# Performance work log

Measured on AMD Instinct MI355X. Metric: run time of the kernel, lower is better.

The kernel has to match this reference:

```python
import jax, jax.numpy as jnp
import numpy as np

WIN = 9


def _box_sum(x, win):
    """Windowed sum over the 3 spatial dims of x: [B,1,D,H,W].

    Separable: three 1-D all-ones convolutions give the exact same sums as the
    original dense win^3 ones-kernel conv, in O(win) per voxel instead of O(win^3).
    """
    pad = win // 2
    for axis in range(3):
        kshape = [1, 1, 1, 1, 1]
        kshape[2 + axis] = win
        kernel = jnp.ones(kshape, x.dtype)
        padding = [(0, 0), (0, 0), (0, 0)]
        padding[axis] = (pad, pad)
        x = jax.lax.conv_general_dilated(
            x, kernel, window_strides=(1, 1, 1), padding=padding,
            dimension_numbers=('NCDHW', 'OIDHW', 'NCDHW'))
    return x


def setup_inputs() -> dict:
    key = jax.random.key(0)
    k1, k2 = jax.random.split(key)
    shape = (2, 1, 160, 192, 160)
    y_true = jax.random.normal(k1, shape, dtype=jnp.float32)
    y_pred = jax.random.normal(k2, shape, dtype=jnp.float32)
    return {"y_true": y_true, "y_pred": y_pred}


def reference(y_true, y_pred):
    Ii, Ji = y_true, y_pred
    win_size = WIN ** 3  # 729

    I_sum = _box_sum(Ii, WIN)
    J_sum = _box_sum(Ji, WIN)
    I2_sum = _box_sum(Ii * Ii, WIN)
    J2_sum = _box_sum(Ji * Ji, WIN)
    IJ_sum = _box_sum(Ii * Ji, WIN)

    u_I = I_sum / win_size
    u_J = J_sum / win_size

    cross = IJ_sum - u_J * I_sum - u_I * J_sum + u_I * u_J * win_size
    I_var = I2_sum - 2.0 * u_I * I_sum + u_I * u_I * win_size
    J_var = J2_sum - 2.0 * u_J * J_sum + u_J * u_J * win_size

    cc = cross * cross / (I_var * J_var + 1e-5)
    # torch: cc.mean(dim=(1,2,3)) per batch (leaves last spatial dim), then -cc.mean()
    cc_b = cc.mean(axis=(1, 2, 3))
    return -cc_b.mean()
```

## Files before the change

kernel.cpp:

```cpp
#include <hip/hip_runtime.h>


#define NB 2
#define ND 160
#define NH 192
#define NW 160
#define TH 16
#define TW 16
#define ZC 32
#define NSTEP (ZC + 8)
#define NSUP (NSTEP / 2)
#define NGRID 1200
#define CPX (NGRID / 8)
#define HROWS 25
#define HSTR 20
#define VROWS 17
#define VSTR 24
#define VFSTR (VROWS * VSTR)
#define NTH 256

#define HSWZ(r) ((((r) >> 3) & 3) << 2)

__device__ __forceinline__ float4 f4add(float4 a, float4 b) {
    return make_float4(a.x + b.x, a.y + b.y, a.z + b.z, a.w + b.w);
}
__device__ __forceinline__ float4 f4sub(float4 a, float4 b) {
    return make_float4(a.x - b.x, a.y - b.y, a.z - b.z, a.w - b.w);
}

__device__ __forceinline__ void barw() {
    asm volatile("s_waitcnt lgkmcnt(0)" ::: "memory");
    __builtin_amdgcn_s_barrier();
    asm volatile("" ::: "memory");
}

__global__ __launch_bounds__(NTH) void ncc_main(
        const float* __restrict__ I, const float* __restrict__ J,
        double* __restrict__ gacc) {
    __shared__ float hsum[2][5][HROWS][HSTR];
    __shared__ float vsum[2][5][VROWS][VSTR];
    __shared__ double wred[4];

    const int tid = threadIdx.x;
    const int tx = tid & 15;
    const int ty = tid >> 4;

    const int bid = blockIdx.x;
    const int nid = (bid & 7) * CPX + (bid >> 3);
    const int tile = nid / 10;
    const int rem = nid - tile * 10;
    const int zci = rem >> 1;
    const int bb = rem & 1;
    const int tileW = tile % 10;
    const int tileH = tile / 10;
    const int w0 = tileW * TW;
    const int h0 = tileH * TH;
    const int z0 = zci * ZC;
    const size_t volBase = (size_t)bb * ND * NH * NW;

    const bool bs_on = (tid < 96);
    const int bp = (bs_on && tid >= 48) ? 1 : 0;
    const int b2 = bs_on ? (tid - bp * 48) : 0;
    const int br = b2 >> 1;
    const int bo = b2 & 1;
    const int bh = h0 - 4 + br;
    const bool h_ok = bs_on && bh >= 0 && bh < NH;
    bool wok[4];
    int goff[4];
#pragma unroll
    for (int kk = 0; kk < 4; ++kk) {
        const int w = w0 - 4 + 8 * bo + 4 * kk;
        wok[kk] = (w >= 0) && (w <= NW - 4);
        goff[kk] = bh * NW + w;
    }
    float bI[16], bJ[16];
#pragma unroll
    for (int k = 0; k < 4; ++k) {
        *(float4*)&bI[4 * k] = make_float4(0.f, 0.f, 0.f, 0.f);
        *(float4*)&bJ[4 * k] = make_float4(0.f, 0.f, 0.f, 0.f);
    }

    const bool c_on = (tid >= 96);
    const int cix = c_on ? (tid - 96) : 0;
    const int cp = (cix >= 80) ? 1 : 0;
    const int c2 = cix - cp * 80;
    const int cf = c2 >> 4;
    const int cstrip = (c2 >> 2) & 3;
    const int ccg = c2 & 3;
    const int cr0 = cstrip << 2;
    const int cc0 = ccg << 2;
    float* cdst = &vsum[cp][cf][cr0][cc0];

#define ISSUE(t) do {                                                          \
    const int zt_ = z0 - 4 + 2 * (t) + bp;                                     \
    const bool zok_ = (zt_ >= 0) && (zt_ < ND);                                \
    const size_t zb_ = volBase + (size_t)zt_ * (NH * NW);                      \
    _Pragma("unroll") for (int kk = 0; kk < 4; ++kk) {                         \
        *(float4*)&bI[4 * kk] = make_float4(0.f, 0.f, 0.f, 0.f);               \
        *(float4*)&bJ[4 * kk] = make_float4(0.f, 0.f, 0.f, 0.f);               \
        if (h_ok && zok_ && wok[kk]) {                                         \
            *(float4*)&bI[4 * kk] = *(const float4*)(I + zb_ + goff[kk]);      \
            *(float4*)&bJ[4 * kk] = *(const float4*)(J + zb_ + goff[kk]);      \
        }                                                                      \
    }                                                                          \
} while (0)

#define BSLIDE(EXPR, F) do {                                                   \
    float s_ = EXPR(0);                                                        \
    _Pragma("unroll") for (int k_ = 1; k_ < 9; ++k_) s_ += EXPR(k_);           \
    float o_[8]; o_[0] = s_;                                                   \
    _Pragma("unroll") for (int j_ = 1; j_ < 8; ++j_) {                         \
        s_ += EXPR(j_ + 8) - EXPR(j_ - 1); o_[j_] = s_; }                      \
    *(float4*)&hsum[bp][F][br][(8 * bo) ^ HSWZ(br)]     = *(float4*)&o_[0];    \
    *(float4*)&hsum[bp][F][br][(8 * bo + 4) ^ HSWZ(br)] = *(float4*)&o_[4];    \
} while (0)
#define E_I(k)  bI[k]
#define E_J(k)  bJ[k]
#define E_I2(k) (bI[k] * bI[k])
#define E_J2(k) (bJ[k] * bJ[k])
#define E_IJ(k) (bI[k] * bJ[k])

#define BSTW() do { if (bs_on) {                                               \
    BSLIDE(E_I, 0); BSLIDE(E_J, 1); BSLIDE(E_I2, 2);                           \
    BSLIDE(E_J2, 3); BSLIDE(E_IJ, 4);                                          \
} } while (0)

#define CRD(r) (*(const float4*)&hsum[cp][cf][r][cc0 ^ HSWZ(r)])

#define DO_C() do { if (c_on) {                                                \
    float4 r0v = CRD(cr0 + 0);                                                 \
    float4 r1v = CRD(cr0 + 1);                                                 \
    float4 r2v = CRD(cr0 + 2);                                                 \
    float4 s4 = f4add(f4add(r0v, r1v), r2v);                                   \
    _Pragma("unroll") for (int k = 3; k < 9; ++k)                              \
        s4 = f4add(s4, CRD(cr0 + k));                                          \
    *(float4*)(cdst + 0 * VSTR) = s4;                                          \
    s4 = f4sub(f4add(s4, CRD(cr0 +  9)), r0v);                                 \
    *(float4*)(cdst + 1 * VSTR) = s4;                                          \
    s4 = f4sub(f4add(s4, CRD(cr0 + 10)), r1v);                                 \
    *(float4*)(cdst + 2 * VSTR) = s4;                                          \
    s4 = f4sub(f4add(s4, CRD(cr0 + 11)), r2v);                                 \
    *(float4*)(cdst + 3 * VSTR) = s4;                                          \
} } while (0)

#define DO_D(PL, SLOT, IDX) do {                                               \
    const float* vbase_ = &vsum[PL][0][ty][tx];                                \
    _Pragma("unroll") for (int f = 0; f < 5; ++f) {                            \
        const float v = vbase_[f * VFSTR];                                     \
        acc[f] += v - ring[f][SLOT];                                           \
        ring[f][SLOT] = v;                                                     \
    }                                                                          \
    if ((IDX) >= 8) {                                                          \
        const float Is = acc[0], Js = acc[1];                                  \
        const float I2 = acc[2], J2 = acc[3], IJ = acc[4];                     \
        const float inv = 1.0f / 729.0f;                                       \
        const float uI = Is * inv, uJ = Js * inv;                              \
        const float cross = IJ - uJ * Is - uI * Js + uI * uJ * 729.0f;         \
        const float Iv = I2 - 2.0f * uI * Is + uI * uI * 729.0f;               \
        const float Jv = J2 - 2.0f * uJ * Js + uJ * uJ * 729.0f;               \
        partial += cross * cross / (Iv * Jv + 1e-5f);                          \
    }                                                                          \
} while (0)

    float ring[5][9];
    float acc[5];
#pragma unroll
    for (int f = 0; f < 5; ++f) {
        acc[f] = 0.f;
#pragma unroll
        for (int k = 0; k < 9; ++k) ring[f][k] = 0.f;
    }
    float partial = 0.f;

    ISSUE(0);
    BSTW();
    ISSUE(1);
    barw();

#pragma unroll 1
    for (int ss = 0; ss < 27; ss += 9) {
#pragma unroll
        for (int jj = 0; jj < 9; ++jj) {
            const int s = ss + jj;
            if (s < NSUP) {
                DO_C();
                barw();

                if (s + 1 < NSUP) BSTW();
                if (s + 2 < NSUP) ISSUE(s + 2);
                DO_D(0, (2 * jj) % 9, 2 * s);
                DO_D(1, (2 * jj + 1) % 9, 2 * s + 1);
                barw();
            }
        }
    }

    double dp = (double)partial;
#pragma unroll
    for (int off = 32; off > 0; off >>= 1)
        dp += __shfl_down(dp, off, 64);
    if ((tid & 63) == 0) wred[tid >> 6] = dp;
    __syncthreads();
    if (tid == 0) atomicAdd(gacc, wred[0] + wred[1] + wred[2] + wred[3]);
}

__global__ void ncc_fin(const double* __restrict__ gacc, float* __restrict__ out) {
    out[0] = (float)(-gacc[0] / (double)((long long)NB * ND * NH * NW));
}

extern "C" void kernel_launch(void* const* d_in, const int* in_sizes, int n_in,
                              void* d_out, int out_size, void* d_ws, size_t ws_size,
                              hipStream_t stream) {
    const float* I = (const float*)d_in[0];
    const float* J = (const float*)d_in[1];
    double* ws = (double*)d_ws;

    hipMemsetAsync(d_ws, 0, sizeof(double), stream);

    ncc_main<<<dim3(NGRID), NTH, 0, stream>>>(I, J, ws);
    ncc_fin<<<1, 1, 0, stream>>>(ws, (float*)d_out);
}
```

Baseline: 91.51 us.

## Switch to single-plane pipeline with smaller z-chunks and more blocks

Replaces the two-plane-per-step pipeline with one z-plane per step. The z-chunk shrinks from 32 to 20 and the grid grows from 1200 to 1920 blocks, so there is more block-level parallelism. In exchange, the 8-plane halo is a larger share of each chunk, so more redundant loads and work, and there are twice as many barriers per plane. It also simplifies the covariance algebra (cross = IJ - uI*Js, etc.), which is mathematically equivalent and saves a few flops.

```diff
diff --git a/kernel.cpp b/kernel.cpp
--- a/kernel.cpp
+++ b/kernel.cpp
@@ -7,10 +7,10 @@
 #define NW 160
 #define TH 16
 #define TW 16
-#define ZC 32
+#define ZC 20
 #define NSTEP (ZC + 8)
-#define NSUP (NSTEP / 2)
-#define NGRID 1200
+#define NITER 36
+#define NGRID 1920
 #define CPX (NGRID / 8)
 #define HROWS 25
 #define HSTR 20
@@ -37,8 +37,8 @@
 __global__ __launch_bounds__(NTH) void ncc_main(
         const float* __restrict__ I, const float* __restrict__ J,
         double* __restrict__ gacc) {
-    __shared__ float hsum[2][5][HROWS][HSTR];
-    __shared__ float vsum[2][5][VROWS][VSTR];
+    __shared__ float hsum[5][HROWS][HSTR];
+    __shared__ float vsum[5][VROWS][VSTR];
     __shared__ double wred[4];
 
     const int tid = threadIdx.x;
@@ -47,8 +47,8 @@
 
     const int bid = blockIdx.x;
     const int nid = (bid & 7) * CPX + (bid >> 3);
-    const int tile = nid / 10;
-    const int rem = nid - tile * 10;
+    const int tile = nid >> 4;
+    const int rem = nid & 15;
     const int zci = rem >> 1;
     const int bb = rem & 1;
     const int tileW = tile % 10;
@@ -58,11 +58,9 @@
     const int z0 = zci * ZC;
     const size_t volBase = (size_t)bb * ND * NH * NW;
 
-    const bool bs_on = (tid < 96);
-    const int bp = (bs_on && tid >= 48) ? 1 : 0;
-    const int b2 = bs_on ? (tid - bp * 48) : 0;
-    const int br = b2 >> 1;
-    const int bo = b2 & 1;
+    const bool bs_on = (tid < 48);
+    const int br = tid >> 1;
+    const int bo = tid & 1;
     const int bh = h0 - 4 + br;
     const bool h_ok = bs_on && bh >= 0 && bh < NH;
     bool wok[4];
@@ -80,19 +78,17 @@
         *(float4*)&bJ[4 * k] = make_float4(0.f, 0.f, 0.f, 0.f);
     }
 
-    const bool c_on = (tid >= 96);
+    const bool c_on = (tid >= 96) && (tid < 176);
     const int cix = c_on ? (tid - 96) : 0;
-    const int cp = (cix >= 80) ? 1 : 0;
-    const int c2 = cix - cp * 80;
-    const int cf = c2 >> 4;
-    const int cstrip = (c2 >> 2) & 3;
-    const int ccg = c2 & 3;
+    const int cf = cix >> 4;
+    const int cstrip = (cix >> 2) & 3;
+    const int ccg = cix & 3;
     const int cr0 = cstrip << 2;
     const int cc0 = ccg << 2;
-    float* cdst = &vsum[cp][cf][cr0][cc0];
+    float* cdst = &vsum[cf][cr0][cc0];
 
 #define ISSUE(t) do {                                                          \
-    const int zt_ = z0 - 4 + 2 * (t) + bp;                                     \
+    const int zt_ = z0 - 4 + (t);                                              \
     const bool zok_ = (zt_ >= 0) && (zt_ < ND);                                \
     const size_t zb_ = volBase + (size_t)zt_ * (NH * NW);                      \
     _Pragma("unroll") for (int kk = 0; kk < 4; ++kk) {                         \
@@ -111,8 +107,8 @@
     float o_[8]; o_[0] = s_;                                                   \
     _Pragma("unroll") for (int j_ = 1; j_ < 8; ++j_) {                         \
         s_ += EXPR(j_ + 8) - EXPR(j_ - 1); o_[j_] = s_; }                      \
-    *(float4*)&hsum[bp][F][br][(8 * bo) ^ HSWZ(br)]     = *(float4*)&o_[0];    \
-    *(float4*)&hsum[bp][F][br][(8 * bo + 4) ^ HSWZ(br)] = *(float4*)&o_[4];    \
+    *(float4*)&hsum[F][br][(8 * bo) ^ HSWZ(br)]     = *(float4*)&o_[0];        \
+    *(float4*)&hsum[F][br][(8 * bo + 4) ^ HSWZ(br)] = *(float4*)&o_[4];        \
 } while (0)
 #define E_I(k)  bI[k]
 #define E_J(k)  bJ[k]
@@ -125,7 +121,7 @@
     BSLIDE(E_J2, 3); BSLIDE(E_IJ, 4);                                          \
 } } while (0)
 
-#define CRD(r) (*(const float4*)&hsum[cp][cf][r][cc0 ^ HSWZ(r)])
+#define CRD(r) (*(const float4*)&hsum[cf][r][cc0 ^ HSWZ(r)])
 
 #define DO_C() do { if (c_on) {                                                \
     float4 r0v = CRD(cr0 + 0);                                                 \
@@ -143,8 +139,8 @@
     *(float4*)(cdst + 3 * VSTR) = s4;                                          \
 } } while (0)
 
-#define DO_D(PL, SLOT, IDX) do {                                               \
-    const float* vbase_ = &vsum[PL][0][ty][tx];                                \
+#define DO_D(SLOT, IDX) do {                                                   \
+    const float* vbase_ = &vsum[0][ty][tx];                                    \
     _Pragma("unroll") for (int f = 0; f < 5; ++f) {                            \
         const float v = vbase_[f * VFSTR];                                     \
         acc[f] += v - ring[f][SLOT];                                           \
@@ -155,9 +151,9 @@
         const float I2 = acc[2], J2 = acc[3], IJ = acc[4];                     \
         const float inv = 1.0f / 729.0f;                                       \
         const float uI = Is * inv, uJ = Js * inv;                              \
-        const float cross = IJ - uJ * Is - uI * Js + uI * uJ * 729.0f;         \
-        const float Iv = I2 - 2.0f * uI * Is + uI * uI * 729.0f;               \
-        const float Jv = J2 - 2.0f * uJ * Js + uJ * uJ * 729.0f;               \
+        const float cross = IJ - uI * Js;                                      \
+        const float Iv = I2 - uI * Is;                                         \
+        const float Jv = J2 - uJ * Js;                                         \
         partial += cross * cross / (Iv * Jv + 1e-5f);                          \
     }                                                                          \
 } while (0)
@@ -178,18 +174,17 @@
     barw();
 
 #pragma unroll 1
-    for (int ss = 0; ss < 27; ss += 9) {
+    for (int ss = 0; ss < NITER; ss += 9) {
 #pragma unroll
         for (int jj = 0; jj < 9; ++jj) {
             const int s = ss + jj;
-            if (s < NSUP) {
+            if (s < NSTEP) {
                 DO_C();
                 barw();
 
-                if (s + 1 < NSUP) BSTW();
-                if (s + 2 < NSUP) ISSUE(s + 2);
-                DO_D(0, (2 * jj) % 9, 2 * s);
-                DO_D(1, (2 * jj + 1) % 9, 2 * s + 1);
+                if (s + 1 < NSTEP) BSTW();
+                if (s + 2 < NSTEP) ISSUE(s + 2);
+                DO_D(jj, s);
                 barw();
             }
         }
```

Measured after the change: 257.2 us. 2.81x slower.

## Spread horizontal box-sum work across all waves, one field per thread

Applied to the files above, without the earlier changes.

The horizontal sliding-sum stage is rebalanced so each of the four waves uses 60 lanes, with every thread handling a single field (I, J, I², J², or (I+J)²) over one 24-wide row. The vertical stage likewise uses 40 lanes per wave instead of dedicated warps. IJ is recovered algebraically as ((I+J)² − I² − J²)/2, and the cross and variance formulas are simplified. This balances the stage work across all waves rather than leaving some waves idle, at the cost of redundant global loads per field and some loss of precision from the polarization identity.

```diff
diff --git a/kernel.cpp b/kernel.cpp
--- a/kernel.cpp
+++ b/kernel.cpp
@@ -10,6 +10,7 @@
 #define ZC 32
 #define NSTEP (ZC + 8)
 #define NSUP (NSTEP / 2)
+#define NITER 27
 #define NGRID 1200
 #define CPX (NGRID / 8)
 #define HROWS 25
@@ -42,6 +43,8 @@
     __shared__ double wred[4];
 
     const int tid = threadIdx.x;
+    const int lane = tid & 63;
+    const int wv = tid >> 6;
     const int tx = tid & 15;
     const int ty = tid >> 4;
 
@@ -58,74 +61,75 @@
     const int z0 = zci * ZC;
     const size_t volBase = (size_t)bb * ND * NH * NW;
 
-    const bool bs_on = (tid < 96);
-    const int bp = (bs_on && tid >= 48) ? 1 : 0;
-    const int b2 = bs_on ? (tid - bp * 48) : 0;
-    const int br = b2 >> 1;
-    const int bo = b2 & 1;
-    const int bh = h0 - 4 + br;
+    const bool bs_on = (lane < 60);
+    const int tk = wv * 60 + (bs_on ? lane : 0);
+    const int bpl = tk / 120;
+    const int bf = (tk / 24) % 5;
+    const int brow = tk % 24;
+    const int bh = h0 - 4 + brow;
     const bool h_ok = bs_on && bh >= 0 && bh < NH;
-    bool wok[4];
-    int goff[4];
-#pragma unroll
-    for (int kk = 0; kk < 4; ++kk) {
-        const int w = w0 - 4 + 8 * bo + 4 * kk;
+    const bool isK = (bf == 4);
+    const float* PA = (bf == 1 || bf == 3) ? J : I;
+    bool wok[6];
+    int goff[6];
+#pragma unroll
+    for (int kk = 0; kk < 6; ++kk) {
+        const int w = w0 - 4 + 4 * kk;
         wok[kk] = (w >= 0) && (w <= NW - 4);
         goff[kk] = bh * NW + w;
     }
-    float bI[16], bJ[16];
-#pragma unroll
-    for (int k = 0; k < 4; ++k) {
-        *(float4*)&bI[4 * k] = make_float4(0.f, 0.f, 0.f, 0.f);
-        *(float4*)&bJ[4 * k] = make_float4(0.f, 0.f, 0.f, 0.f);
-    }
-
-    const bool c_on = (tid >= 96);
-    const int cix = c_on ? (tid - 96) : 0;
-    const int cp = (cix >= 80) ? 1 : 0;
-    const int c2 = cix - cp * 80;
+    float bR[24];
+#pragma unroll
+    for (int k = 0; k < 6; ++k) *(float4*)&bR[4 * k] = make_float4(0.f, 0.f, 0.f, 0.f);
+
+    const bool c_on = (lane < 40);
+    const int cix = wv * 40 + (c_on ? lane : 0);
+    const int cpl = (cix >= 80) ? 1 : 0;
+    const int c2 = cix - cpl * 80;
     const int cf = c2 >> 4;
     const int cstrip = (c2 >> 2) & 3;
     const int ccg = c2 & 3;
     const int cr0 = cstrip << 2;
     const int cc0 = ccg << 2;
-    float* cdst = &vsum[cp][cf][cr0][cc0];
+    float* cdst = &vsum[cpl][cf][cr0][cc0];
 
 #define ISSUE(t) do {                                                          \
-    const int zt_ = z0 - 4 + 2 * (t) + bp;                                     \
+    const int zt_ = z0 - 4 + 2 * (t) + bpl;                                    \
     const bool zok_ = (zt_ >= 0) && (zt_ < ND);                                \
     const size_t zb_ = volBase + (size_t)zt_ * (NH * NW);                      \
-    _Pragma("unroll") for (int kk = 0; kk < 4; ++kk) {                         \
-        *(float4*)&bI[4 * kk] = make_float4(0.f, 0.f, 0.f, 0.f);               \
-        *(float4*)&bJ[4 * kk] = make_float4(0.f, 0.f, 0.f, 0.f);               \
+    _Pragma("unroll") for (int kk = 0; kk < 6; ++kk) {                         \
+        float4 q = make_float4(0.f, 0.f, 0.f, 0.f);                            \
         if (h_ok && zok_ && wok[kk]) {                                         \
-            *(float4*)&bI[4 * kk] = *(const float4*)(I + zb_ + goff[kk]);      \
-            *(float4*)&bJ[4 * kk] = *(const float4*)(J + zb_ + goff[kk]);      \
+            q = *(const float4*)(PA + zb_ + goff[kk]);                         \
+            if (isK) {                                                         \
+                float4 q2 = *(const float4*)(J + zb_ + goff[kk]);              \
+                q = f4add(q, q2);                                              \
+            }                                                                  \
         }                                                                      \
+        *(float4*)&bR[4 * kk] = q;                                             \
     }                                                                          \
 } while (0)
 
-#define BSLIDE(EXPR, F) do {                                                   \
-    float s_ = EXPR(0);                                                        \
-    _Pragma("unroll") for (int k_ = 1; k_ < 9; ++k_) s_ += EXPR(k_);           \
-    float o_[8]; o_[0] = s_;                                                   \
-    _Pragma("unroll") for (int j_ = 1; j_ < 8; ++j_) {                         \
-        s_ += EXPR(j_ + 8) - EXPR(j_ - 1); o_[j_] = s_; }                      \
-    *(float4*)&hsum[bp][F][br][(8 * bo) ^ HSWZ(br)]     = *(float4*)&o_[0];    \
-    *(float4*)&hsum[bp][F][br][(8 * bo + 4) ^ HSWZ(br)] = *(float4*)&o_[4];    \
-} while (0)
-#define E_I(k)  bI[k]
-#define E_J(k)  bJ[k]
-#define E_I2(k) (bI[k] * bI[k])
-#define E_J2(k) (bJ[k] * bJ[k])
-#define E_IJ(k) (bI[k] * bJ[k])
-
 #define BSTW() do { if (bs_on) {                                               \
-    BSLIDE(E_I, 0); BSLIDE(E_J, 1); BSLIDE(E_I2, 2);                           \
-    BSLIDE(E_J2, 3); BSLIDE(E_IJ, 4);                                          \
+    float p[24];                                                               \
+    _Pragma("unroll") for (int k = 0; k < 24; ++k) {                           \
+        const float m = (bf < 2) ? 1.0f : bR[k];                               \
+        p[k] = bR[k] * m;                                                      \
+    }                                                                          \
+    float s = p[0];                                                            \
+    _Pragma("unroll") for (int k = 1; k < 9; ++k) s += p[k];                   \
+    float* hrow = &hsum[bpl][bf][brow][0];                                     \
+    _Pragma("unroll") for (int g = 0; g < 4; ++g) {                            \
+        float4 ov; ov.x = s;                                                   \
+        s += p[g * 4 + 9]  - p[g * 4 + 0]; ov.y = s;                           \
+        s += p[g * 4 + 10] - p[g * 4 + 1]; ov.z = s;                           \
+        s += p[g * 4 + 11] - p[g * 4 + 2]; ov.w = s;                           \
+        *(float4*)(hrow + ((4 * g) ^ HSWZ(brow))) = ov;                        \
+        if (g < 3) s += p[g * 4 + 12] - p[g * 4 + 3];                          \
+    }                                                                          \
 } } while (0)
 
-#define CRD(r) (*(const float4*)&hsum[cp][cf][r][cc0 ^ HSWZ(r)])
+#define CRD(r) (*(const float4*)&hsum[cpl][cf][r][cc0 ^ HSWZ(r)])
 
 #define DO_C() do { if (c_on) {                                                \
     float4 r0v = CRD(cr0 + 0);                                                 \
@@ -152,12 +156,13 @@
     }                                                                          \
     if ((IDX) >= 8) {                                                          \
         const float Is = acc[0], Js = acc[1];                                  \
-        const float I2 = acc[2], J2 = acc[3], IJ = acc[4];                     \
+        const float I2 = acc[2], J2 = acc[3], K2 = acc[4];                     \
+        const float IJ = 0.5f * (K2 - I2 - J2);                                \
         const float inv = 1.0f / 729.0f;                                       \
         const float uI = Is * inv, uJ = Js * inv;                              \
-        const float cross = IJ - uJ * Is - uI * Js + uI * uJ * 729.0f;         \
-        const float Iv = I2 - 2.0f * uI * Is + uI * uI * 729.0f;               \
-        const float Jv = J2 - 2.0f * uJ * Js + uJ * uJ * 729.0f;               \
+        const float cross = IJ - uI * Js;                                      \
+        const float Iv = I2 - uI * Is;                                         \
+        const float Jv = J2 - uJ * Js;                                         \
         partial += cross * cross / (Iv * Jv + 1e-5f);                          \
     }                                                                          \
 } while (0)
@@ -178,7 +183,7 @@
     barw();
 
 #pragma unroll 1
-    for (int ss = 0; ss < 27; ss += 9) {
+    for (int ss = 0; ss < NITER; ss += 9) {
 #pragma unroll
         for (int jj = 0; jj < 9; ++jj) {
             const int s = ss + jj;
```

Result: slower. 145.1 us (+58.5%).

## Spread horizontal box-sum over 192 threads, interleave vsum layout, simplify NCC algebra

Applied to the files above, without the earlier changes.

The horizontal sliding-sum stage now uses 192 threads, each handling 4 output columns from 12 loaded floats, instead of 96 threads handling 8 columns from 16 floats. This shortens the serial per-thread work and register footprint on the critical path, but loads more overlapping halo data. The vsum shared array is reordered to [plane][row][field][col], which changes the stride and bank pattern of the per-thread field reads. The cross/variance formulas are algebraically simplified to drop redundant multiplies. Threads 96-191 now do both the horizontal stage and the column stage, which may lengthen their share of each step.

```diff
diff --git a/kernel.cpp b/kernel.cpp
--- a/kernel.cpp
+++ b/kernel.cpp
@@ -10,13 +10,14 @@
 #define ZC 32
 #define NSTEP (ZC + 8)
 #define NSUP (NSTEP / 2)
+#define NITER 27
 #define NGRID 1200
 #define CPX (NGRID / 8)
 #define HROWS 25
 #define HSTR 20
 #define VROWS 17
 #define VSTR 24
-#define VFSTR (VROWS * VSTR)
+#define VRSTR (5 * VSTR)
 #define NTH 256
 
 #define HSWZ(r) ((((r) >> 3) & 3) << 2)
@@ -38,7 +39,7 @@
         const float* __restrict__ I, const float* __restrict__ J,
         double* __restrict__ gacc) {
     __shared__ float hsum[2][5][HROWS][HSTR];
-    __shared__ float vsum[2][5][VROWS][VSTR];
+    __shared__ float vsum[2][VROWS][5][VSTR];
     __shared__ double wred[4];
 
     const int tid = threadIdx.x;
@@ -58,44 +59,44 @@
     const int z0 = zci * ZC;
     const size_t volBase = (size_t)bb * ND * NH * NW;
 
-    const bool bs_on = (tid < 96);
-    const int bp = (bs_on && tid >= 48) ? 1 : 0;
-    const int b2 = bs_on ? (tid - bp * 48) : 0;
-    const int br = b2 >> 1;
-    const int bo = b2 & 1;
+    const bool bs_on = (tid < 192);
+    const int bpl = (bs_on && tid >= 96) ? 1 : 0;
+    const int b2 = bs_on ? (tid - bpl * 96) : 0;
+    const int br = b2 >> 2;
+    const int bq = b2 & 3;
     const int bh = h0 - 4 + br;
     const bool h_ok = bs_on && bh >= 0 && bh < NH;
-    bool wok[4];
-    int goff[4];
-#pragma unroll
-    for (int kk = 0; kk < 4; ++kk) {
-        const int w = w0 - 4 + 8 * bo + 4 * kk;
+    bool wok[3];
+    int goff[3];
+#pragma unroll
+    for (int kk = 0; kk < 3; ++kk) {
+        const int w = w0 - 4 + 4 * bq + 4 * kk;
         wok[kk] = (w >= 0) && (w <= NW - 4);
         goff[kk] = bh * NW + w;
     }
-    float bI[16], bJ[16];
-#pragma unroll
-    for (int k = 0; k < 4; ++k) {
+    float bI[12], bJ[12];
+#pragma unroll
+    for (int k = 0; k < 3; ++k) {
         *(float4*)&bI[4 * k] = make_float4(0.f, 0.f, 0.f, 0.f);
         *(float4*)&bJ[4 * k] = make_float4(0.f, 0.f, 0.f, 0.f);
     }
 
     const bool c_on = (tid >= 96);
     const int cix = c_on ? (tid - 96) : 0;
-    const int cp = (cix >= 80) ? 1 : 0;
-    const int c2 = cix - cp * 80;
+    const int cpl = (cix >= 80) ? 1 : 0;
+    const int c2 = cix - cpl * 80;
     const int cf = c2 >> 4;
     const int cstrip = (c2 >> 2) & 3;
     const int ccg = c2 & 3;
     const int cr0 = cstrip << 2;
     const int cc0 = ccg << 2;
-    float* cdst = &vsum[cp][cf][cr0][cc0];
+    float* cdst = &vsum[cpl][cr0][cf][cc0];
 
 #define ISSUE(t) do {                                                          \
-    const int zt_ = z0 - 4 + 2 * (t) + bp;                                     \
+    const int zt_ = z0 - 4 + 2 * (t) + bpl;                                    \
     const bool zok_ = (zt_ >= 0) && (zt_ < ND);                                \
     const size_t zb_ = volBase + (size_t)zt_ * (NH * NW);                      \
-    _Pragma("unroll") for (int kk = 0; kk < 4; ++kk) {                         \
+    _Pragma("unroll") for (int kk = 0; kk < 3; ++kk) {                         \
         *(float4*)&bI[4 * kk] = make_float4(0.f, 0.f, 0.f, 0.f);               \
         *(float4*)&bJ[4 * kk] = make_float4(0.f, 0.f, 0.f, 0.f);               \
         if (h_ok && zok_ && wok[kk]) {                                         \
@@ -108,11 +109,10 @@
 #define BSLIDE(EXPR, F) do {                                                   \
     float s_ = EXPR(0);                                                        \
     _Pragma("unroll") for (int k_ = 1; k_ < 9; ++k_) s_ += EXPR(k_);           \
-    float o_[8]; o_[0] = s_;                                                   \
-    _Pragma("unroll") for (int j_ = 1; j_ < 8; ++j_) {                         \
+    float o_[4]; o_[0] = s_;                                                   \
+    _Pragma("unroll") for (int j_ = 1; j_ < 4; ++j_) {                         \
         s_ += EXPR(j_ + 8) - EXPR(j_ - 1); o_[j_] = s_; }                      \
-    *(float4*)&hsum[bp][F][br][(8 * bo) ^ HSWZ(br)]     = *(float4*)&o_[0];    \
-    *(float4*)&hsum[bp][F][br][(8 * bo + 4) ^ HSWZ(br)] = *(float4*)&o_[4];    \
+    *(float4*)&hsum[bpl][F][br][(4 * bq) ^ HSWZ(br)] = *(float4*)&o_[0];       \
 } while (0)
 #define E_I(k)  bI[k]
 #define E_J(k)  bJ[k]
@@ -125,7 +125,7 @@
     BSLIDE(E_J2, 3); BSLIDE(E_IJ, 4);                                          \
 } } while (0)
 
-#define CRD(r) (*(const float4*)&hsum[cp][cf][r][cc0 ^ HSWZ(r)])
+#define CRD(r) (*(const float4*)&hsum[cpl][cf][r][cc0 ^ HSWZ(r)])
 
 #define DO_C() do { if (c_on) {                                                \
     float4 r0v = CRD(cr0 + 0);                                                 \
@@ -134,19 +134,19 @@
     float4 s4 = f4add(f4add(r0v, r1v), r2v);                                   \
     _Pragma("unroll") for (int k = 3; k < 9; ++k)                              \
         s4 = f4add(s4, CRD(cr0 + k));                                          \
-    *(float4*)(cdst + 0 * VSTR) = s4;                                          \
+    *(float4*)(cdst + 0 * VRSTR) = s4;                                         \
     s4 = f4sub(f4add(s4, CRD(cr0 +  9)), r0v);                                 \
-    *(float4*)(cdst + 1 * VSTR) = s4;                                          \
+    *(float4*)(cdst + 1 * VRSTR) = s4;                                         \
     s4 = f4sub(f4add(s4, CRD(cr0 + 10)), r1v);                                 \
-    *(float4*)(cdst + 2 * VSTR) = s4;                                          \
+    *(float4*)(cdst + 2 * VRSTR) = s4;                                         \
     s4 = f4sub(f4add(s4, CRD(cr0 + 11)), r2v);                                 \
-    *(float4*)(cdst + 3 * VSTR) = s4;                                          \
+    *(float4*)(cdst + 3 * VRSTR) = s4;                                         \
 } } while (0)
 
 #define DO_D(PL, SLOT, IDX) do {                                               \
-    const float* vbase_ = &vsum[PL][0][ty][tx];                                \
+    const float* vbase_ = &vsum[PL][ty][0][tx];                                \
     _Pragma("unroll") for (int f = 0; f < 5; ++f) {                            \
-        const float v = vbase_[f * VFSTR];                                     \
+        const float v = vbase_[f * VSTR];                                      \
         acc[f] += v - ring[f][SLOT];                                           \
         ring[f][SLOT] = v;                                                     \
     }                                                                          \
@@ -155,9 +155,9 @@
         const float I2 = acc[2], J2 = acc[3], IJ = acc[4];                     \
         const float inv = 1.0f / 729.0f;                                       \
         const float uI = Is * inv, uJ = Js * inv;                              \
-        const float cross = IJ - uJ * Is - uI * Js + uI * uJ * 729.0f;         \
-        const float Iv = I2 - 2.0f * uI * Is + uI * uI * 729.0f;               \
-        const float Jv = J2 - 2.0f * uJ * Js + uJ * uJ * 729.0f;               \
+        const float cross = IJ - uI * Js;                                      \
+        const float Iv = I2 - uI * Is;                                         \
+        const float Jv = J2 - uJ * Js;                                         \
         partial += cross * cross / (Iv * Jv + 1e-5f);                          \
     }                                                                          \
 } while (0)
@@ -178,7 +178,7 @@
     barw();
 
 #pragma unroll 1
-    for (int ss = 0; ss < 27; ss += 9) {
+    for (int ss = 0; ss < NITER; ss += 9) {
 #pragma unroll
         for (int jj = 0; jj < 9; ++jj) {
             const int s = ss + jj;
```

New measurement: 78.51 us (median of 2 runs). -14.2%, faster.
